# Kernel optimization log

Hardware: AMD Instinct MI355X
Metric: run time of the kernel (lower is better)

## Reference

```python
import jax, jax.numpy as jnp
import numpy as np

TOP_K = 4
NORM_P = 1.0  # moe_normalize_expert_weights


def setup_inputs() -> dict:
    key = jax.random.key(0)
    k1, k2 = jax.random.split(key)
    hidden_states = jax.random.normal(k1, (4, 2048, 6144), dtype=jnp.float32)
    router_weight = jax.random.normal(k2, (16, 6144), dtype=jnp.float32) * 0.02
    return {"hidden_states": hidden_states, "router_weight": router_weight}


def reference(hidden_states, router_weight):
    # flatten tokens: [B, S, H] -> [T, H]
    x = hidden_states.reshape(-1, hidden_states.shape[-1])
    # rowwise linear (no bias): logits [T, E]
    logits = jnp.einsum('th,eh->te', x, router_weight)
    probs = jax.nn.softmax(logits, axis=-1)
    top_weights, top_experts = jax.lax.top_k(probs, TOP_K)
    # p-norm rescaling (p=1 -> sum of abs)
    scale = jnp.sum(jnp.abs(top_weights) ** NORM_P, axis=-1, keepdims=True) ** (1.0 / NORM_P)
    top_weights = top_weights / scale
    return top_weights, top_experts
```

## Files before the change

### kernel.cpp

```cpp
#include <hip/hip_runtime.h>
#include <math.h>
#include <stdint.h>


constexpr int H       = 6144;
constexpr int E       = 16;
constexpr int HC      = 256;
constexpr int NCH     = H / HC;
constexpr int TPB     = 256;
constexpr int TOK_PB  = 16;
constexpr int T_TOTAL = 8192;

__device__ __forceinline__ void gll16(const float* g, float* l) {
    __builtin_amdgcn_global_load_lds(
        (const __attribute__((address_space(1))) uint32_t*)g,
        (__attribute__((address_space(3))) uint32_t*)l,
        16, 0, 0);
}

__global__ __launch_bounds__(TPB, 2)
void dbrx_router(const float* __restrict__ x,
                 const float* __restrict__ w,
                 float* __restrict__ out)
{
    __shared__ float wlds[3][E * HC];
    __shared__ float lred[4][64];

    const int tid  = threadIdx.x;
    const int wave = tid >> 6;
    const int lane = tid & 63;
    const int tok0 = blockIdx.x * TOK_PB + wave * 4;

    const float* xptr = x + (size_t)tok0 * H + lane * 4;

    float acc[64];
    #pragma unroll
    for (int i = 0; i < 64; ++i) acc[i] = 0.f;

    float4 xa[4], xf[4], xg[4];

#define ISSUE(C, B, XV) do {                                           \
        _Pragma("unroll")                                              \
        for (int j = 0; j < 4; ++j)                                    \
            gll16(w + (size_t)(j * 4 + wave) * H + (C) * HC + lane * 4,\
                  &wlds[B][(j * 4 + wave) * HC]);                      \
        _Pragma("unroll")                                              \
        for (int t = 0; t < 4; ++t)                                    \
            XV[t] = *reinterpret_cast<const float4*>(                  \
                xptr + (size_t)t * H + (C) * HC);                      \
    } while (0)

#define COMPUTE(B, XV) do {                                            \
        _Pragma("unroll")                                              \
        for (int eb = 0; eb < 4; ++eb) {                               \
            float4 wv[4];                                              \
            _Pragma("unroll")                                          \
            for (int e = 0; e < 4; ++e)                                \
                wv[e] = *reinterpret_cast<const float4*>(              \
                    &wlds[B][(eb * 4 + e) * HC + lane * 4]);           \
            _Pragma("unroll")                                          \
            for (int t = 0; t < 4; ++t)                                \
                _Pragma("unroll")                                      \
                for (int e = 0; e < 4; ++e) {                          \
                    float s = acc[t * 16 + eb * 4 + e];                \
                    s = fmaf(XV[t].x, wv[e].x, s);                     \
                    s = fmaf(XV[t].y, wv[e].y, s);                     \
                    s = fmaf(XV[t].z, wv[e].z, s);                     \
                    s = fmaf(XV[t].w, wv[e].w, s);                     \
                    acc[t * 16 + eb * 4 + e] = s;                      \
                }                                                      \
        }                                                              \
    } while (0)

#define STEPBAR(NV) do {                                               \
        asm volatile("s_waitcnt vmcnt(" #NV ") lgkmcnt(0)" ::: "memory"); \
        __builtin_amdgcn_s_barrier();                                  \
    } while (0)

    ISSUE(0, 0, xa);
    ISSUE(1, 1, xf);

    for (int cc = 0; cc < 21; cc += 3) {
        STEPBAR(8); COMPUTE(0, xa); ISSUE(cc + 2, 2, xg);
        STEPBAR(8); COMPUTE(1, xf); ISSUE(cc + 3, 0, xa);
        STEPBAR(8); COMPUTE(2, xg); ISSUE(cc + 4, 1, xf);
    }
    STEPBAR(8); COMPUTE(0, xa); ISSUE(23, 2, xg);
    STEPBAR(8); COMPUTE(1, xf);
    STEPBAR(0); COMPUTE(2, xg);
#undef ISSUE
#undef COMPUTE
#undef STEPBAR

#define RSTEP(S) do {                                                  \
        constexpr int HN = 32 >> (S);                                  \
        const bool hi = (lane & HN) != 0;                              \
        _Pragma("unroll")                                              \
        for (int i = 0; i < HN; ++i) {                                 \
            float send = hi ? acc[i] : acc[i + HN];                    \
            float keep = hi ? acc[i + HN] : acc[i];                    \
            float recv = __shfl_xor(send, HN, 64);                     \
            acc[i] = keep + recv;                                      \
        }                                                              \
    } while (0)
    RSTEP(0); RSTEP(1); RSTEP(2); RSTEP(3); RSTEP(4); RSTEP(5);
#undef RSTEP

    lred[wave][lane] = acc[0];
    __syncthreads();

    if (tid < TOK_PB) {
        float lg[16];
        #pragma unroll
        for (int e = 0; e < 16; ++e)
            lg[e] = lred[tid >> 2][(tid & 3) * 16 + e];

        float topv[4];
        int   topi[4];
        #pragma unroll
        for (int k = 0; k < 4; ++k) {
            float m = lg[0]; int mi = 0;
            #pragma unroll
            for (int e = 1; e < 16; ++e)
                if (lg[e] > m) { m = lg[e]; mi = e; }
            topv[k] = m; topi[k] = mi;
            #pragma unroll
            for (int e = 0; e < 16; ++e)
                if (e == mi) lg[e] = -INFINITY;
        }

        float ex[4]; float sum = 0.f;
        #pragma unroll
        for (int k = 0; k < 4; ++k) { ex[k] = __expf(topv[k] - topv[0]); sum += ex[k]; }
        const float inv = 1.0f / sum;

        const int tok = blockIdx.x * TOK_PB + tid;
        #pragma unroll
        for (int k = 0; k < 4; ++k) {
            out[(size_t)tok * 4 + k] = ex[k] * inv;
            out[(size_t)T_TOTAL * 4 + (size_t)tok * 4 + k] = (float)topi[k];
        }
    }
}

extern "C" void kernel_launch(void* const* d_in, const int* in_sizes, int n_in,
                              void* d_out, int out_size, void* d_ws, size_t ws_size,
                              hipStream_t stream) {
    const float* x = (const float*)d_in[0];
    const float* w = (const float*)d_in[1];
    float* out     = (float*)d_out;
    dbrx_router<<<T_TOTAL / TOK_PB, TPB, 0, stream>>>(x, w, out);
}
```

Baseline: 40.87 us.

## Split weight and activation prefetch and use a four-deep LDS ring

Weight chunks now stream into a four-buffer LDS ring and are issued two chunks ahead, right after each barrier and before the compute step. Activation registers are double-buffered, one chunk ahead, instead of triple-buffered. The compute loop is regrouped into eight expert pairs, and the remainder steps are guarded by conditionals rather than an explicit epilogue. The aim is to free registers and keep the weight loads hidden, at the cost of more LDS per block and shallower prefetching of the activation stream, which dominates memory traffic.

After: 156.5 us. +283.1%, slower.

```diff
diff --git a/kernel.cpp b/kernel.cpp
--- a/kernel.cpp
+++ b/kernel.cpp
@@ -7,6 +7,7 @@
 constexpr int E       = 16;
 constexpr int HC      = 256;
 constexpr int NCH     = H / HC;
+constexpr int NBUF    = 4;
 constexpr int TPB     = 256;
 constexpr int TOK_PB  = 16;
 constexpr int T_TOTAL = 8192;
@@ -23,7 +24,7 @@
                  const float* __restrict__ w,
                  float* __restrict__ out)
 {
-    __shared__ float wlds[3][E * HC];
+    __shared__ float wlds[NBUF][E * HC];
     __shared__ float lred[4][64];
 
     const int tid  = threadIdx.x;
@@ -37,13 +38,16 @@
     #pragma unroll
     for (int i = 0; i < 64; ++i) acc[i] = 0.f;
 
-    float4 xa[4], xf[4], xg[4];
+    float4 xa[4], xf[4];
 
-#define ISSUE(C, B, XV) do {                                           \
+#define ISSUE_W(C, B) do {                                             \
         _Pragma("unroll")                                              \
         for (int j = 0; j < 4; ++j)                                    \
             gll16(w + (size_t)(j * 4 + wave) * H + (C) * HC + lane * 4,\
                   &wlds[B][(j * 4 + wave) * HC]);                      \
+    } while (0)
+
+#define ISSUE_X(C, XV) do {                                            \
         _Pragma("unroll")                                              \
         for (int t = 0; t < 4; ++t)                                    \
             XV[t] = *reinterpret_cast<const float4*>(                  \
@@ -52,43 +56,55 @@
 
 #define COMPUTE(B, XV) do {                                            \
         _Pragma("unroll")                                              \
-        for (int eb = 0; eb < 4; ++eb) {                               \
-            float4 wv[4];                                              \
+        for (int eb = 0; eb < 8; ++eb) {                               \
+            float4 wv[2];                                              \
             _Pragma("unroll")                                          \
-            for (int e = 0; e < 4; ++e)                                \
+            for (int e = 0; e < 2; ++e)                                \
                 wv[e] = *reinterpret_cast<const float4*>(              \
-                    &wlds[B][(eb * 4 + e) * HC + lane * 4]);           \
+                    &wlds[B][(eb * 2 + e) * HC + lane * 4]);           \
             _Pragma("unroll")                                          \
             for (int t = 0; t < 4; ++t)                                \
                 _Pragma("unroll")                                      \
-                for (int e = 0; e < 4; ++e) {                          \
-                    float s = acc[t * 16 + eb * 4 + e];                \
+                for (int e = 0; e < 2; ++e) {                          \
+                    float s = acc[t * 16 + eb * 2 + e];                \
                     s = fmaf(XV[t].x, wv[e].x, s);                     \
                     s = fmaf(XV[t].y, wv[e].y, s);                     \
                     s = fmaf(XV[t].z, wv[e].z, s);                     \
                     s = fmaf(XV[t].w, wv[e].w, s);                     \
-                    acc[t * 16 + eb * 4 + e] = s;                      \
+                    acc[t * 16 + eb * 2 + e] = s;                      \
                 }                                                      \
         }                                                              \
     } while (0)
 
-#define STEPBAR(NV) do {                                               \
-        asm volatile("s_waitcnt vmcnt(" #NV ") lgkmcnt(0)" ::: "memory"); \
+#define STEPBAR() do {                                                 \
+        asm volatile("s_waitcnt vmcnt(8) lgkmcnt(0)" ::: "memory");    \
         __builtin_amdgcn_s_barrier();                                  \
     } while (0)
 
-    ISSUE(0, 0, xa);
-    ISSUE(1, 1, xf);
+    ISSUE_W(0, 0);
+    ISSUE_W(1, 1);
+    ISSUE_X(0, xa);
 
-    for (int cc = 0; cc < 21; cc += 3) {
-        STEPBAR(8); COMPUTE(0, xa); ISSUE(cc + 2, 2, xg);
-        STEPBAR(8); COMPUTE(1, xf); ISSUE(cc + 3, 0, xa);
-        STEPBAR(8); COMPUTE(2, xg); ISSUE(cc + 4, 1, xf);
+    for (int cc = 0; cc < NCH; cc += 4) {
+        STEPBAR();
+        if (cc + 2 < NCH) ISSUE_W(cc + 2, 2);
+        COMPUTE(0, xa);
+        ISSUE_X(cc + 1, xf);
+        STEPBAR();
+        if (cc + 3 < NCH) ISSUE_W(cc + 3, 3);
+        COMPUTE(1, xf);
+        if (cc + 2 < NCH) ISSUE_X(cc + 2, xa);
+        STEPBAR();
+        if (cc + 4 < NCH) ISSUE_W(cc + 4, 0);
+        COMPUTE(2, xa);
+        if (cc + 3 < NCH) ISSUE_X(cc + 3, xf);
+        STEPBAR();
+        if (cc + 5 < NCH) ISSUE_W(cc + 5, 1);
+        COMPUTE(3, xf);
+        if (cc + 4 < NCH) ISSUE_X(cc + 4, xa);
     }
-    STEPBAR(8); COMPUTE(0, xa); ISSUE(23, 2, xg);
-    STEPBAR(8); COMPUTE(1, xf);
-    STEPBAR(0); COMPUTE(2, xg);
-#undef ISSUE
+#undef ISSUE_W
+#undef ISSUE_X
 #undef COMPUTE
 #undef STEPBAR
 
```
